# Kernel tuning notes

Measured on AMD Instinct MI355X. Metric: run time of the kernel, lower is better.

Reference implementation:

```python
import jax, jax.numpy as jnp
import numpy as np

N_SPECIES = 4
NUM_MODELS = 8
LAYER_DIMS = [384, 160, 128, 96, 1]
CELU_ALPHA = 0.1
N_ATOMS = 50000  # divisible by N_SPECIES -> balanced routing


def setup_inputs() -> dict:
    key = jax.random.key(0)
    ks = jax.random.split(key, 2 + 2 * (len(LAYER_DIMS) - 1))
    # Balanced species assignment: exactly N_ATOMS/N_SPECIES atoms per species,
    # randomly permuted (mirrors a real molecule's scattered per-species atoms
    # while keeping per-species group sizes static for jit).
    base = jnp.tile(jnp.arange(N_SPECIES, dtype=jnp.int64), N_ATOMS // N_SPECIES)
    species = jax.random.permutation(ks[0], base)[None, :]  # [1, N_ATOMS]
    aev = jax.random.normal(ks[1], (1, N_ATOMS, LAYER_DIMS[0]), dtype=jnp.float32)
    inp = {"species": species, "aev": aev}
    # Fused ensemble params per species: W [S, M, in, out], b [S, M, 1, out]
    for li in range(len(LAYER_DIMS) - 1):
        fin, fout = LAYER_DIMS[li], LAYER_DIMS[li + 1]
        scale = 1.0 / np.sqrt(fin)
        inp[f"W{li+1}"] = jax.random.uniform(
            ks[2 + 2 * li], (N_SPECIES, NUM_MODELS, fin, fout),
            dtype=jnp.float32, minval=-scale, maxval=scale)
        inp[f"b{li+1}"] = jax.random.uniform(
            ks[3 + 2 * li], (N_SPECIES, NUM_MODELS, 1, fout),
            dtype=jnp.float32, minval=-scale, maxval=scale)
    return inp


def _ensemble_mlp(x, W1, b1, W2, b2, W3, b3, W4, b4):
    # x: [S, n, F] routed atoms per species; W: [S, M, fin, fout]; b: [S, M, 1, fout]
    celu = lambda h: jax.nn.celu(h, alpha=CELU_ALPHA)
    h = celu(jnp.einsum('snf,smfo->smno', x, W1) + b1)   # [S, M, n, 160]
    h = celu(jnp.einsum('smnf,smfo->smno', h, W2) + b2)  # [S, M, n, 128]
    h = celu(jnp.einsum('smnf,smfo->smno', h, W3) + b3)  # [S, M, n, 96]
    h = jnp.einsum('smnf,smfo->smno', h, W4) + b4        # [S, M, n, 1]
    return h.mean(axis=1)                                 # mean over models -> [S, n, 1]


def reference(species, aev, W1, b1, W2, b2, W3, b3, W4, b4):
    n_atoms = species.shape[1]
    n_per = n_atoms // N_SPECIES
    # species-routed gather: stable argsort groups atoms by species; counts are
    # static (balanced) so reshape into [S, n_per] groups (== per-species index_select)
    order = jnp.argsort(species.reshape(-1), stable=True)
    x = aev.reshape(n_atoms, -1)[order].reshape(N_SPECIES, n_per, -1)
    atom_e = _ensemble_mlp(x, W1, b1, W2, b2, W3, b3, W4, b4)  # [S, n_per, 1]
    mol_energies = jnp.sum(atom_e).reshape(1)  # scatter-sum over all atoms/species
    return mol_energies
```

## Files before the change

kernel.cpp:

```cpp
#include <hip/hip_runtime.h>


#define NSP 4
#define NMODELS 8
#define MSPLIT 2
#define MPB (NMODELS / MSPLIT)
#define NATOMS 50000
#define NPER (NATOMS / NSP)
#define D0 384
#define D1 160
#define D2 128
#define D3 96
#define NRBLK ((NATOMS + 255) / 256)
#define ABLK 128
#define BPS ((NPER + ABLK - 1) / ABLK)
#define FRAGS_SM 184
#define CHUNKS_M 23
#define TOT_CHUNKS (MPB * CHUNKS_M)

typedef float f32x4 __attribute__((ext_vector_type(4)));
typedef __bf16 bf16x8 __attribute__((ext_vector_type(8)));

#define MFMA16(a, b, c) __builtin_amdgcn_mfma_f32_16x16x32_bf16((a), (b), (c), 0, 0, 0)

#define PALL_BYTES ((size_t)NSP * NMODELS * FRAGS_SM * 1024)
#define PBIAS_OFF PALL_BYTES
#define PBIAS_BYTES ((size_t)NSP * NMODELS * 512 * 2)
#define ORDER_OFF (PBIAS_OFF + PBIAS_BYTES)
#define BCNT_OFF (ORDER_OFF + (size_t)NATOMS * 4)
#define BPFX_OFF (BCNT_OFF + (size_t)NRBLK * NSP * 4)
#define BASE_OFF (BPFX_OFF + (size_t)NRBLK * NSP * 4)

static __device__ __forceinline__ unsigned short bfbits(float f) {
  __bf16 h = (__bf16)f;
  return __builtin_bit_cast(unsigned short, h);
}

static __device__ __forceinline__ float celu01(float x) {
  return fmaxf(x, 0.f) + 0.1f * fminf(0.f, __expf(x * 10.f) - 1.f);
}

static __device__ __forceinline__ void gload16(const void* g, void* l) {
  __builtin_amdgcn_global_load_lds(
      (const __attribute__((address_space(1))) unsigned int*)g,
      (__attribute__((address_space(3))) unsigned int*)l, 16, 0, 0);
}

__global__ __launch_bounds__(256) void count_kernel(const int* __restrict__ species,
                                                    int* __restrict__ bcnt) {
  __shared__ int cnt[NSP];
  int t = threadIdx.x;
  if (t < NSP) cnt[t] = 0;
  __syncthreads();
  int i = blockIdx.x * 256 + t;
  if (i < NATOMS) atomicAdd(&cnt[species[i]], 1);
  __syncthreads();
  if (t < NSP) bcnt[blockIdx.x * NSP + t] = cnt[t];
}

__global__ __launch_bounds__(256) void scan_kernel(const int* __restrict__ bcnt,
                                                   int* __restrict__ bpfx,
                                                   int* __restrict__ base) {
  int w = threadIdx.x >> 6;
  int lane = threadIdx.x & 63;
  __shared__ int totals[NSP];
  int carry = 0;
  for (int c = 0; c < (NRBLK + 63) / 64; ++c) {
    int idx = c * 64 + lane;
    int v = (idx < NRBLK) ? bcnt[idx * NSP + w] : 0;
    int incl = v;
    for (int off = 1; off < 64; off <<= 1) {
      int tv = __shfl_up(incl, off);
      if (lane >= off) incl += tv;
    }
    if (idx < NRBLK) bpfx[idx * NSP + w] = carry + incl - v;
    carry += __shfl(incl, 63);
  }
  if (lane == 0) totals[w] = carry;
  __syncthreads();
  if (threadIdx.x == 0) {
    int run = 0;
    for (int s = 0; s < NSP; ++s) { base[s] = run; run += totals[s]; }
  }
}

__global__ __launch_bounds__(256) void route_kernel(const int* __restrict__ species,
                                                    const int* __restrict__ bpfx,
                                                    const int* __restrict__ base,
                                                    int* __restrict__ order) {
  __shared__ int sp[256];
  int t = threadIdx.x;
  int i = blockIdx.x * 256 + t;
  sp[t] = (i < NATOMS) ? species[i] : -1;
  __syncthreads();
  if (i < NATOMS) {
    int s = sp[t];
    int rank = 0;
    for (int j = 0; j < t; ++j) rank += (sp[j] == s) ? 1 : 0;
    order[base[s] + bpfx[blockIdx.x * NSP + s] + rank] = i;
  }
}

__global__ __launch_bounds__(256) void pack_kernel(const float* __restrict__ W,
                                                   unsigned* __restrict__ dst,
                                                   int K, int N, int NT, int fragBase,
                                                   int total) {
  int tid = blockIdx.x * 256 + threadIdx.x;
  if (tid >= total) return;
  int per_sm = K * N / 2;
  int smi = tid / per_sm;
  int rem = tid - smi * per_sm;
  int frag = rem >> 8;
  int wi = rem & 255;
  int l = wi >> 2, d = wi & 3;
  int kf = frag / NT;
  int nt = frag - kf * NT;
  int k = kf * 32 + ((l >> 4) << 3) + 2 * d;
  int n = nt * 16 + (l & 15);
  const float* p = W + ((size_t)smi * K + k) * N + n;
  unsigned lo = bfbits(p[0]);
  unsigned hi = bfbits(p[N]);
  dst[((size_t)smi * FRAGS_SM + fragBase + frag) * 256 + wi] = lo | (hi << 16);
}

__global__ __launch_bounds__(256) void param_pack(const float* __restrict__ b1,
                                                  const float* __restrict__ b2,
                                                  const float* __restrict__ b3,
                                                  const float* __restrict__ W4,
                                                  const float* __restrict__ b4,
                                                  unsigned short* __restrict__ dst) {
  int i = blockIdx.x * 256 + threadIdx.x;
  if (i >= NSP * NMODELS * 512) return;
  int smi = i >> 9, o = i & 511;
  unsigned short v = 0;
  if (o < 160) v = bfbits(b1[smi * 160 + o]);
  else if (o < 288) v = bfbits(b2[smi * 128 + (o - 160)]);
  else if (o < 384) v = bfbits(b3[smi * 96 + (o - 288)]);
  else if (o < 480) v = bfbits(W4[smi * 96 + (o - 384)]);
  else if (o < 482) {
    unsigned u = __builtin_bit_cast(unsigned, b4[smi]);
    v = (unsigned short)((o == 480) ? (u & 0xffffu) : (u >> 16));
  }
  dst[i] = v;
}

__global__ __launch_bounds__(256, 2) void mlp_kernel(
    const float* __restrict__ aev, const int* __restrict__ order,
    const unsigned short* __restrict__ pAll, const unsigned short* __restrict__ pPar,
    float* __restrict__ out) {
  __shared__ alignas(16) unsigned short stage[2][4096];
  __shared__ alignas(16) __bf16 hbuf[4][32][168];
  __shared__ alignas(16) unsigned short hpar[MPB * 512];

  const int nwg = NSP * BPS * MSPLIT;
  const int cpx = nwg / 8;
  const int blk = (blockIdx.x % 8) * cpx + blockIdx.x / 8;
  const int s = blk / (BPS * MSPLIT);
  const int rem = blk - s * (BPS * MSPLIT);
  const int mh = rem / BPS;
  const int sb = rem - mh * BPS;
  const int tid = threadIdx.x;
  const int w = tid >> 6;
  const int l = tid & 63;
  const int l15 = l & 15;
  const int l4 = l >> 4;

  {
    const int4* src = (const int4*)(pPar + ((size_t)(s * NMODELS + mh * MPB)) * 512);
    ((int4*)hpar)[tid] = src[tid];
  }

  const size_t smBase = (size_t)(s * NMODELS + mh * MPB) * FRAGS_SM;
  const char* wsrc = (const char*)pAll + smBase * 1024 + (size_t)w * 2048 + (size_t)l * 16;

  bf16x8 a1[2][12];
#pragma unroll
  for (int mt = 0; mt < 2; ++mt) {
    int slot = sb * ABLK + w * 32 + mt * 16 + l15;
    int g = (slot < NPER) ? order[s * NPER + slot] : -1;
    if (g >= 0) {
      const float* rp = aev + (size_t)g * D0 + l4 * 8;
#pragma unroll
      for (int kf = 0; kf < 12; ++kf) {
        const float4* q = (const float4*)(rp + kf * 32);
        float4 lo = q[0], hi = q[1];
        bf16x8 f;
        f[0] = (__bf16)lo.x; f[1] = (__bf16)lo.y; f[2] = (__bf16)lo.z; f[3] = (__bf16)lo.w;
        f[4] = (__bf16)hi.x; f[5] = (__bf16)hi.y; f[6] = (__bf16)hi.z; f[7] = (__bf16)hi.w;
        a1[mt][kf] = f;
      }
    } else {
#pragma unroll
      for (int kf = 0; kf < 12; ++kf) {
        bf16x8 z;
#pragma unroll
        for (int e = 0; e < 8; ++e) z[e] = (__bf16)0.f;
        a1[mt][kf] = z;
      }
    }
  }

  const __bf16* hb = (const __bf16*)hpar;
  float acc4[2][4] = {{0.f, 0.f, 0.f, 0.f}, {0.f, 0.f, 0.f, 0.f}};
  float bbacc = 0.f;

  {
    char* d = (char*)stage + w * 2048;
    gload16(wsrc, d);
    gload16(wsrc + 1024, d + 1024);
  }
  __syncthreads();

  auto stage_next = [&](int gn) {
    if (gn < TOT_CHUNKS) {
      char* d = (char*)stage + (gn & 1) * 8192 + w * 2048;
      const char* src = wsrc + (size_t)gn * 8192;
      gload16(src, d);
      gload16(src + 1024, d + 1024);
    }
  };

  int gc = 0;

#pragma unroll 1
  for (int m = 0; m < MPB; ++m) {
    f32x4 C[2][10];

#pragma unroll
    for (int mt = 0; mt < 2; ++mt)
#pragma unroll
      for (int nt = 0; nt < 10; ++nt) {
        f32x4 z; z[0] = z[1] = z[2] = z[3] = 0.f; C[mt][nt] = z;
      }
#pragma unroll
    for (int c = 0; c < 15; ++c) {
      stage_next(gc + 1);
      const bf16x8* sbuf = (const bf16x8*)((const char*)stage + (gc & 1) * 8192);
#pragma unroll
      for (int j = 0; j < 8; ++j) {
        const int f = c * 8 + j;
        bf16x8 b = sbuf[j * 64 + l];
        C[0][f % 10] = MFMA16(a1[0][f / 10], b, C[0][f % 10]);
        C[1][f % 10] = MFMA16(a1[1][f / 10], b, C[1][f % 10]);
      }
      __syncthreads();
      ++gc;
    }
#pragma unroll
    for (int nt = 0; nt < 10; ++nt) {
      float bias = (float)hb[m * 512 + nt * 16 + l15];
#pragma unroll
      for (int mt = 0; mt < 2; ++mt)
#pragma unroll
        for (int r = 0; r < 4; ++r)
          hbuf[w][mt * 16 + l4 * 4 + r][nt * 16 + l15] = (__bf16)celu01(C[mt][nt][r] + bias);
    }

    bf16x8 a2[2][5];
#pragma unroll
    for (int mt = 0; mt < 2; ++mt)
#pragma unroll
      for (int kf = 0; kf < 5; ++kf)
        a2[mt][kf] = *(const bf16x8*)&hbuf[w][mt * 16 + l15][kf * 32 + l4 * 8];

#pragma unroll
    for (int mt = 0; mt < 2; ++mt)
#pragma unroll
      for (int nt = 0; nt < 8; ++nt) {
        f32x4 z; z[0] = z[1] = z[2] = z[3] = 0.f; C[mt][nt] = z;
      }
#pragma unroll
    for (int lc = 0; lc < 5; ++lc) {
      stage_next(gc + 1);
      const bf16x8* sbuf = (const bf16x8*)((const char*)stage + (gc & 1) * 8192);
#pragma unroll
      for (int j = 0; j < 8; ++j) {
        bf16x8 b = sbuf[j * 64 + l];
        C[0][j] = MFMA16(a2[0][lc], b, C[0][j]);
        C[1][j] = MFMA16(a2[1][lc], b, C[1][j]);
      }
      __syncthreads();
      ++gc;
    }
#pragma unroll
    for (int nt = 0; nt < 8; ++nt) {
      float bias = (float)hb[m * 512 + 160 + nt * 16 + l15];
#pragma unroll
      for (int mt = 0; mt < 2; ++mt)
#pragma unroll
        for (int r = 0; r < 4; ++r)
          hbuf[w][mt * 16 + l4 * 4 + r][nt * 16 + l15] = (__bf16)celu01(C[mt][nt][r] + bias);
    }

    bf16x8 a3[2][4];
#pragma unroll
    for (int mt = 0; mt < 2; ++mt)
#pragma unroll
      for (int kf = 0; kf < 4; ++kf)
        a3[mt][kf] = *(const bf16x8*)&hbuf[w][mt * 16 + l15][kf * 32 + l4 * 8];

#pragma unroll
    for (int mt = 0; mt < 2; ++mt)
#pragma unroll
      for (int nt = 0; nt < 6; ++nt) {
        f32x4 z; z[0] = z[1] = z[2] = z[3] = 0.f; C[mt][nt] = z;
      }
#pragma unroll
    for (int lc = 0; lc < 3; ++lc) {
      stage_next(gc + 1);
      const bf16x8* sbuf = (const bf16x8*)((const char*)stage + (gc & 1) * 8192);
#pragma unroll
      for (int j = 0; j < 8; ++j) {
        const int f = lc * 8 + j;
        bf16x8 b = sbuf[j * 64 + l];
        C[0][f % 6] = MFMA16(a3[0][f / 6], b, C[0][f % 6]);
        C[1][f % 6] = MFMA16(a3[1][f / 6], b, C[1][f % 6]);
      }
      __syncthreads();
      ++gc;
    }

    float e[2][4] = {{0.f, 0.f, 0.f, 0.f}, {0.f, 0.f, 0.f, 0.f}};
#pragma unroll
    for (int nt = 0; nt < 6; ++nt) {
      float b3v = (float)hb[m * 512 + 288 + nt * 16 + l15];
      float w4v = (float)hb[m * 512 + 384 + nt * 16 + l15];
#pragma unroll
      for (int mt = 0; mt < 2; ++mt)
#pragma unroll
        for (int r = 0; r < 4; ++r)
          e[mt][r] += celu01(C[mt][nt][r] + b3v) * w4v;
    }
#pragma unroll
    for (int mt = 0; mt < 2; ++mt)
#pragma unroll
      for (int r = 0; r < 4; ++r) acc4[mt][r] += e[mt][r];
    bbacc += ((const float*)hpar)[m * 256 + 240];
  }

  float tot = 0.f;
#pragma unroll
  for (int mt = 0; mt < 2; ++mt)
#pragma unroll
    for (int r = 0; r < 4; ++r) {
      float v = acc4[mt][r];
      v += __shfl_xor(v, 1);
      v += __shfl_xor(v, 2);
      v += __shfl_xor(v, 4);
      v += __shfl_xor(v, 8);
      int slot = sb * ABLK + w * 32 + mt * 16 + l4 * 4 + r;
      if (l15 == 0 && slot < NPER) tot += v + bbacc;
    }
  tot *= (1.f / NMODELS);
#pragma unroll
  for (int off = 1; off < 64; off <<= 1) tot += __shfl_xor(tot, off);
  if (l == 0) atomicAdd(out, tot);
}

extern "C" void kernel_launch(void* const* d_in, const int* in_sizes, int n_in,
                              void* d_out, int out_size, void* d_ws, size_t ws_size,
                              hipStream_t stream) {
  (void)in_sizes; (void)n_in; (void)out_size; (void)ws_size;
  const int* species = (const int*)d_in[0];
  const float* aev = (const float*)d_in[1];
  const float* W1 = (const float*)d_in[2];
  const float* b1 = (const float*)d_in[3];
  const float* W2 = (const float*)d_in[4];
  const float* b2 = (const float*)d_in[5];
  const float* W3 = (const float*)d_in[6];
  const float* b3 = (const float*)d_in[7];
  const float* W4 = (const float*)d_in[8];
  const float* b4 = (const float*)d_in[9];
  float* out = (float*)d_out;
  char* ws = (char*)d_ws;

  unsigned short* pAll = (unsigned short*)ws;
  unsigned short* pPar = (unsigned short*)(ws + PBIAS_OFF);
  int* order = (int*)(ws + ORDER_OFF);
  int* bcnt = (int*)(ws + BCNT_OFF);
  int* bpfx = (int*)(ws + BPFX_OFF);
  int* base = (int*)(ws + BASE_OFF);

  hipMemsetAsync(d_out, 0, sizeof(float), stream);

  count_kernel<<<NRBLK, 256, 0, stream>>>(species, bcnt);
  scan_kernel<<<1, 256, 0, stream>>>(bcnt, bpfx, base);
  route_kernel<<<NRBLK, 256, 0, stream>>>(species, bpfx, base, order);

  {
    int total = NSP * NMODELS * D0 * D1 / 2;
    pack_kernel<<<(total + 255) / 256, 256, 0, stream>>>(W1, (unsigned*)pAll, D0, D1, D1 / 16, 0, total);
  }
  {
    int total = NSP * NMODELS * D1 * D2 / 2;
    pack_kernel<<<(total + 255) / 256, 256, 0, stream>>>(W2, (unsigned*)pAll, D1, D2, D2 / 16, 120, total);
  }
  {
    int total = NSP * NMODELS * D2 * D3 / 2;
    pack_kernel<<<(total + 255) / 256, 256, 0, stream>>>(W3, (unsigned*)pAll, D2, D3, D3 / 16, 160, total);
  }
  {
    int total = NSP * NMODELS * 512;
    param_pack<<<(total + 255) / 256, 256, 0, stream>>>(b1, b2, b3, W4, b4, pPar);
  }

  mlp_kernel<<<NSP * BPS * MSPLIT, 256, 0, stream>>>(aev, order, pAll, pPar, out);
}
```

Baseline: 226.1 us.

## Split each layer's output columns in halves to cut registers and raise occupancy

Each layer's matmul is now computed in two passes over halves of the output columns. This halves the accumulator register footprint, so launch bounds can ask for 3 workgroups per CU instead of 2. The weight staging chunk is halved (4 KB double buffer) and the weights are repacked per column-half to match, doubling the chunk count and the number of barriers. The LDS copy of bias and params is removed in favour of direct global loads, which trades LDS space for extra scattered global reads. More launches of the pack kernel are also added.

```diff
diff --git a/kernel.cpp b/kernel.cpp
--- a/kernel.cpp
+++ b/kernel.cpp
@@ -15,7 +15,7 @@
 #define ABLK 128
 #define BPS ((NPER + ABLK - 1) / ABLK)
 #define FRAGS_SM 184
-#define CHUNKS_M 23
+#define CHUNKS_M 46
 #define TOT_CHUNKS (MPB * CHUNKS_M)
 
 typedef float f32x4 __attribute__((ext_vector_type(4)));
@@ -103,11 +103,12 @@
 
 __global__ __launch_bounds__(256) void pack_kernel(const float* __restrict__ W,
                                                    unsigned* __restrict__ dst,
-                                                   int K, int N, int NT, int fragBase,
+                                                   int K, int Nstride, int NT,
+                                                   int colBase, int fragBase,
                                                    int total) {
   int tid = blockIdx.x * 256 + threadIdx.x;
   if (tid >= total) return;
-  int per_sm = K * N / 2;
+  int per_sm = K * NT * 8;
   int smi = tid / per_sm;
   int rem = tid - smi * per_sm;
   int frag = rem >> 8;
@@ -116,10 +117,10 @@
   int kf = frag / NT;
   int nt = frag - kf * NT;
   int k = kf * 32 + ((l >> 4) << 3) + 2 * d;
-  int n = nt * 16 + (l & 15);
-  const float* p = W + ((size_t)smi * K + k) * N + n;
+  int n = colBase + nt * 16 + (l & 15);
+  const float* p = W + ((size_t)smi * K + k) * Nstride + n;
   unsigned lo = bfbits(p[0]);
-  unsigned hi = bfbits(p[N]);
+  unsigned hi = bfbits(p[Nstride]);
   dst[((size_t)smi * FRAGS_SM + fragBase + frag) * 256 + wi] = lo | (hi << 16);
 }
 
@@ -144,13 +145,12 @@
   dst[i] = v;
 }
 
-__global__ __launch_bounds__(256, 2) void mlp_kernel(
+__global__ __launch_bounds__(256, 3) void mlp_kernel(
     const float* __restrict__ aev, const int* __restrict__ order,
     const unsigned short* __restrict__ pAll, const unsigned short* __restrict__ pPar,
     float* __restrict__ out) {
-  __shared__ alignas(16) unsigned short stage[2][4096];
+  __shared__ alignas(16) unsigned short stage[2][2048];
   __shared__ alignas(16) __bf16 hbuf[4][32][168];
-  __shared__ alignas(16) unsigned short hpar[MPB * 512];
 
   const int nwg = NSP * BPS * MSPLIT;
   const int cpx = nwg / 8;
@@ -165,13 +165,13 @@
   const int l15 = l & 15;
   const int l4 = l >> 4;
 
-  {
-    const int4* src = (const int4*)(pPar + ((size_t)(s * NMODELS + mh * MPB)) * 512);
-    ((int4*)hpar)[tid] = src[tid];
-  }
-
   const size_t smBase = (size_t)(s * NMODELS + mh * MPB) * FRAGS_SM;
-  const char* wsrc = (const char*)pAll + smBase * 1024 + (size_t)w * 2048 + (size_t)l * 16;
+  const char* wsrc = (const char*)pAll + smBase * 1024 + (size_t)w * 1024 + (size_t)l * 16;
+
+  const unsigned short* parBf = pPar + (size_t)(s * NMODELS + mh * MPB) * 512;
+  auto ldbf = [&](int off) -> float {
+    return (float)__builtin_bit_cast(__bf16, parBf[off]);
+  };
 
   bf16x8 a1[2][12];
 #pragma unroll
@@ -200,60 +200,55 @@
     }
   }
 
-  const __bf16* hb = (const __bf16*)hpar;
   float acc4[2][4] = {{0.f, 0.f, 0.f, 0.f}, {0.f, 0.f, 0.f, 0.f}};
   float bbacc = 0.f;
 
-  {
-    char* d = (char*)stage + w * 2048;
-    gload16(wsrc, d);
-    gload16(wsrc + 1024, d + 1024);
-  }
+  gload16(wsrc, (char*)stage + w * 1024);
   __syncthreads();
 
   auto stage_next = [&](int gn) {
-    if (gn < TOT_CHUNKS) {
-      char* d = (char*)stage + (gn & 1) * 8192 + w * 2048;
-      const char* src = wsrc + (size_t)gn * 8192;
-      gload16(src, d);
-      gload16(src + 1024, d + 1024);
-    }
+    if (gn < TOT_CHUNKS)
+      gload16(wsrc + (size_t)gn * 4096,
+              (char*)stage + ((gn & 1) << 12) + w * 1024);
   };
 
   int gc = 0;
 
 #pragma unroll 1
   for (int m = 0; m < MPB; ++m) {
-    f32x4 C[2][10];
-
-#pragma unroll
-    for (int mt = 0; mt < 2; ++mt)
-#pragma unroll
-      for (int nt = 0; nt < 10; ++nt) {
-        f32x4 z; z[0] = z[1] = z[2] = z[3] = 0.f; C[mt][nt] = z;
-      }
-#pragma unroll
-    for (int c = 0; c < 15; ++c) {
-      stage_next(gc + 1);
-      const bf16x8* sbuf = (const bf16x8*)((const char*)stage + (gc & 1) * 8192);
-#pragma unroll
-      for (int j = 0; j < 8; ++j) {
-        const int f = c * 8 + j;
-        bf16x8 b = sbuf[j * 64 + l];
-        C[0][f % 10] = MFMA16(a1[0][f / 10], b, C[0][f % 10]);
-        C[1][f % 10] = MFMA16(a1[1][f / 10], b, C[1][f % 10]);
-      }
-      __syncthreads();
-      ++gc;
-    }
-#pragma unroll
-    for (int nt = 0; nt < 10; ++nt) {
-      float bias = (float)hb[m * 512 + nt * 16 + l15];
+#pragma unroll 1
+    for (int p = 0; p < 2; ++p) {
+      f32x4 C[2][5];
 #pragma unroll
       for (int mt = 0; mt < 2; ++mt)
 #pragma unroll
-        for (int r = 0; r < 4; ++r)
-          hbuf[w][mt * 16 + l4 * 4 + r][nt * 16 + l15] = (__bf16)celu01(C[mt][nt][r] + bias);
+        for (int nt = 0; nt < 5; ++nt) {
+          f32x4 z; z[0] = z[1] = z[2] = z[3] = 0.f; C[mt][nt] = z;
+        }
+#pragma unroll
+      for (int c = 0; c < 15; ++c) {
+        stage_next(gc + 1);
+        const bf16x8* sbuf = (const bf16x8*)((const char*)stage + ((gc & 1) << 12));
+#pragma unroll
+        for (int j = 0; j < 4; ++j) {
+          const int f = c * 4 + j;
+          bf16x8 b = sbuf[j * 64 + l];
+          C[0][f % 5] = MFMA16(a1[0][f / 5], b, C[0][f % 5]);
+          C[1][f % 5] = MFMA16(a1[1][f / 5], b, C[1][f % 5]);
+        }
+        __syncthreads();
+        ++gc;
+      }
+#pragma unroll
+      for (int nt = 0; nt < 5; ++nt) {
+        float bias = ldbf(m * 512 + p * 80 + nt * 16 + l15);
+#pragma unroll
+        for (int mt = 0; mt < 2; ++mt)
+#pragma unroll
+          for (int r = 0; r < 4; ++r)
+            hbuf[w][mt * 16 + l4 * 4 + r][p * 80 + nt * 16 + l15] =
+                (__bf16)celu01(C[mt][nt][r] + bias);
+      }
     }
 
     bf16x8 a2[2][5];
@@ -263,33 +258,39 @@
       for (int kf = 0; kf < 5; ++kf)
         a2[mt][kf] = *(const bf16x8*)&hbuf[w][mt * 16 + l15][kf * 32 + l4 * 8];
 
-#pragma unroll
-    for (int mt = 0; mt < 2; ++mt)
-#pragma unroll
-      for (int nt = 0; nt < 8; ++nt) {
-        f32x4 z; z[0] = z[1] = z[2] = z[3] = 0.f; C[mt][nt] = z;
-      }
-#pragma unroll
-    for (int lc = 0; lc < 5; ++lc) {
-      stage_next(gc + 1);
-      const bf16x8* sbuf = (const bf16x8*)((const char*)stage + (gc & 1) * 8192);
-#pragma unroll
-      for (int j = 0; j < 8; ++j) {
-        bf16x8 b = sbuf[j * 64 + l];
-        C[0][j] = MFMA16(a2[0][lc], b, C[0][j]);
-        C[1][j] = MFMA16(a2[1][lc], b, C[1][j]);
-      }
-      __syncthreads();
-      ++gc;
-    }
-#pragma unroll
-    for (int nt = 0; nt < 8; ++nt) {
-      float bias = (float)hb[m * 512 + 160 + nt * 16 + l15];
+#pragma unroll 1
+    for (int p = 0; p < 2; ++p) {
+      f32x4 C[2][4];
 #pragma unroll
       for (int mt = 0; mt < 2; ++mt)
 #pragma unroll
-        for (int r = 0; r < 4; ++r)
-          hbuf[w][mt * 16 + l4 * 4 + r][nt * 16 + l15] = (__bf16)celu01(C[mt][nt][r] + bias);
+        for (int nt = 0; nt < 4; ++nt) {
+          f32x4 z; z[0] = z[1] = z[2] = z[3] = 0.f; C[mt][nt] = z;
+        }
+#pragma unroll
+      for (int c = 0; c < 5; ++c) {
+        stage_next(gc + 1);
+        const bf16x8* sbuf = (const bf16x8*)((const char*)stage + ((gc & 1) << 12));
+#pragma unroll
+        for (int j = 0; j < 4; ++j) {
+          const int f = c * 4 + j;
+          bf16x8 b = sbuf[j * 64 + l];
+          C[0][f % 4] = MFMA16(a2[0][f / 4], b, C[0][f % 4]);
+          C[1][f % 4] = MFMA16(a2[1][f / 4], b, C[1][f % 4]);
+        }
+        __syncthreads();
+        ++gc;
+      }
+#pragma unroll
+      for (int nt = 0; nt < 4; ++nt) {
+        float bias = ldbf(m * 512 + 160 + p * 64 + nt * 16 + l15);
+#pragma unroll
+        for (int mt = 0; mt < 2; ++mt)
+#pragma unroll
+          for (int r = 0; r < 4; ++r)
+            hbuf[w][mt * 16 + l4 * 4 + r][p * 64 + nt * 16 + l15] =
+                (__bf16)celu01(C[mt][nt][r] + bias);
+      }
     }
 
     bf16x8 a3[2][4];
@@ -299,43 +300,46 @@
       for (int kf = 0; kf < 4; ++kf)
         a3[mt][kf] = *(const bf16x8*)&hbuf[w][mt * 16 + l15][kf * 32 + l4 * 8];
 
+    float e[2][4] = {{0.f, 0.f, 0.f, 0.f}, {0.f, 0.f, 0.f, 0.f}};
+#pragma unroll 1
+    for (int p = 0; p < 2; ++p) {
+      f32x4 C[2][3];
+#pragma unroll
+      for (int mt = 0; mt < 2; ++mt)
+#pragma unroll
+        for (int nt = 0; nt < 3; ++nt) {
+          f32x4 z; z[0] = z[1] = z[2] = z[3] = 0.f; C[mt][nt] = z;
+        }
+#pragma unroll
+      for (int c = 0; c < 3; ++c) {
+        stage_next(gc + 1);
+        const bf16x8* sbuf = (const bf16x8*)((const char*)stage + ((gc & 1) << 12));
+#pragma unroll
+        for (int j = 0; j < 4; ++j) {
+          const int f = c * 4 + j;
+          bf16x8 b = sbuf[j * 64 + l];
+          C[0][f % 3] = MFMA16(a3[0][f / 3], b, C[0][f % 3]);
+          C[1][f % 3] = MFMA16(a3[1][f / 3], b, C[1][f % 3]);
+        }
+        __syncthreads();
+        ++gc;
+      }
+#pragma unroll
+      for (int nt = 0; nt < 3; ++nt) {
+        float b3v = ldbf(m * 512 + 288 + p * 48 + nt * 16 + l15);
+        float w4v = ldbf(m * 512 + 384 + p * 48 + nt * 16 + l15);
+#pragma unroll
+        for (int mt = 0; mt < 2; ++mt)
+#pragma unroll
+          for (int r = 0; r < 4; ++r)
+            e[mt][r] += celu01(C[mt][nt][r] + b3v) * w4v;
+      }
+    }
 #pragma unroll
     for (int mt = 0; mt < 2; ++mt)
 #pragma unroll
-      for (int nt = 0; nt < 6; ++nt) {
-        f32x4 z; z[0] = z[1] = z[2] = z[3] = 0.f; C[mt][nt] = z;
-      }
-#pragma unroll
-    for (int lc = 0; lc < 3; ++lc) {
-      stage_next(gc + 1);
-      const bf16x8* sbuf = (const bf16x8*)((const char*)stage + (gc & 1) * 8192);
-#pragma unroll
-      for (int j = 0; j < 8; ++j) {
-        const int f = lc * 8 + j;
-        bf16x8 b = sbuf[j * 64 + l];
-        C[0][f % 6] = MFMA16(a3[0][f / 6], b, C[0][f % 6]);
-        C[1][f % 6] = MFMA16(a3[1][f / 6], b, C[1][f % 6]);
-      }
-      __syncthreads();
-      ++gc;
-    }
-
-    float e[2][4] = {{0.f, 0.f, 0.f, 0.f}, {0.f, 0.f, 0.f, 0.f}};
-#pragma unroll
-    for (int nt = 0; nt < 6; ++nt) {
-      float b3v = (float)hb[m * 512 + 288 + nt * 16 + l15];
-      float w4v = (float)hb[m * 512 + 384 + nt * 16 + l15];
-#pragma unroll
-      for (int mt = 0; mt < 2; ++mt)
-#pragma unroll
-        for (int r = 0; r < 4; ++r)
-          e[mt][r] += celu01(C[mt][nt][r] + b3v) * w4v;
-    }
-#pragma unroll
-    for (int mt = 0; mt < 2; ++mt)
-#pragma unroll
       for (int r = 0; r < 4; ++r) acc4[mt][r] += e[mt][r];
-    bbacc += ((const float*)hpar)[m * 256 + 240];
+    bbacc += ((const float*)pPar)[(size_t)(s * NMODELS + mh * MPB + m) * 256 + 240];
   }
 
   float tot = 0.f;
@@ -388,16 +392,19 @@
   route_kernel<<<NRBLK, 256, 0, stream>>>(species, bpfx, base, order);
 
   {
-    int total = NSP * NMODELS * D0 * D1 / 2;
-    pack_kernel<<<(total + 255) / 256, 256, 0, stream>>>(W1, (unsigned*)pAll, D0, D1, D1 / 16, 0, total);
+    int total = NSP * NMODELS * D0 * 80 / 2;
+    pack_kernel<<<(total + 255) / 256, 256, 0, stream>>>(W1, (unsigned*)pAll, D0, D1, 5, 0, 0, total);
+    pack_kernel<<<(total + 255) / 256, 256, 0, stream>>>(W1, (unsigned*)pAll, D0, D1, 5, 80, 60, total);
   }
   {
-    int total = NSP * NMODELS * D1 * D2 / 2;
-    pack_kernel<<<(total + 255) / 256, 256, 0, stream>>>(W2, (unsigned*)pAll, D1, D2, D2 / 16, 120, total);
+    int total = NSP * NMODELS * D1 * 64 / 2;
+    pack_kernel<<<(total + 255) / 256, 256, 0, stream>>>(W2, (unsigned*)pAll, D1, D2, 4, 0, 120, total);
+    pack_kernel<<<(total + 255) / 256, 256, 0, stream>>>(W2, (unsigned*)pAll, D1, D2, 4, 64, 140, total);
   }
   {
-    int total = NSP * NMODELS * D2 * D3 / 2;
-    pack_kernel<<<(total + 255) / 256, 256, 0, stream>>>(W3, (unsigned*)pAll, D2, D3, D3 / 16, 160, total);
+    int total = NSP * NMODELS * D2 * 48 / 2;
+    pack_kernel<<<(total + 255) / 256, 256, 0, stream>>>(W3, (unsigned*)pAll, D2, D3, 3, 0, 160, total);
+    pack_kernel<<<(total + 255) / 256, 256, 0, stream>>>(W3, (unsigned*)pAll, D2, D3, 3, 48, 172, total);
   }
   {
     int total = NSP * NMODELS * 512;
```

After: 317.5 us. +40.4%, slower.

## Swap MFMA operands to pass activations via register shuffles and prepack AEV

Applied to the files above, without the earlier changes.

The MLP kernel now treats weights as the A operand and activations as the B operand. Inter-layer activations are redistributed with wave shuffles instead of round-tripping through an LDS buffer. A new pre-kernel gathers the routed AEV rows into bf16 MFMA-fragment layout, so the main kernel streams layer-1 activations per K-fragment instead of holding all 12 in registers. Dropping the LDS hbuf and hpar and cutting register pressure allows 3 blocks per CU instead of 2. The cost is an extra gather kernel, a workspace round trip for AEV, and bias reads from global memory.

```diff
diff --git a/kernel.cpp b/kernel.cpp
--- a/kernel.cpp
+++ b/kernel.cpp
@@ -7,6 +7,8 @@
 #define MPB (NMODELS / MSPLIT)
 #define NATOMS 50000
 #define NPER (NATOMS / NSP)
+#define NPAD 12544
+#define NG16 (NPAD / 16)
 #define D0 384
 #define D1 160
 #define D2 128
@@ -17,6 +19,7 @@
 #define FRAGS_SM 184
 #define CHUNKS_M 23
 #define TOT_CHUNKS (MPB * CHUNKS_M)
+#define MAXKF(c) ((8 * (c) + 7) / 10)
 
 typedef float f32x4 __attribute__((ext_vector_type(4)));
 typedef __bf16 bf16x8 __attribute__((ext_vector_type(8)));
@@ -30,10 +33,16 @@
 #define BCNT_OFF (ORDER_OFF + (size_t)NATOMS * 4)
 #define BPFX_OFF (BCNT_OFF + (size_t)NRBLK * NSP * 4)
 #define BASE_OFF (BPFX_OFF + (size_t)NRBLK * NSP * 4)
+#define AEVF_OFF (BASE_OFF + 1024)
+#define AEVF_BYTES ((size_t)NSP * NG16 * 12 * 1024)
 
 static __device__ __forceinline__ unsigned short bfbits(float f) {
   __bf16 h = (__bf16)f;
   return __builtin_bit_cast(unsigned short, h);
+}
+
+static __device__ __forceinline__ float bf2f(unsigned short u) {
+  return (float)__builtin_bit_cast(__bf16, u);
 }
 
 static __device__ __forceinline__ float celu01(float x) {
@@ -99,6 +108,33 @@
     for (int j = 0; j < t; ++j) rank += (sp[j] == s) ? 1 : 0;
     order[base[s] + bpfx[blockIdx.x * NSP + s] + rank] = i;
   }
+}
+
+__global__ __launch_bounds__(256) void aev_pack(const float* __restrict__ aev,
+                                                const int* __restrict__ order,
+                                                unsigned short* __restrict__ aevf) {
+  int tid = blockIdx.x * 256 + threadIdx.x;
+  int frag = tid >> 6;
+  int l = tid & 63;
+  if (frag >= NSP * NG16 * 12) return;
+  int s = frag / (NG16 * 12);
+  int r2 = frag - s * (NG16 * 12);
+  int g16 = r2 / 12;
+  int kf = r2 - g16 * 12;
+  int slot = g16 * 16 + (l & 15);
+  int k0 = kf * 32 + (l >> 4) * 8;
+  unsigned short o[8];
+  if (slot < NPER) {
+    int src = order[s * NPER + slot];
+    const float4* q = (const float4*)(aev + (size_t)src * D0 + k0);
+    float4 v0 = q[0], v1 = q[1];
+    o[0] = bfbits(v0.x); o[1] = bfbits(v0.y); o[2] = bfbits(v0.z); o[3] = bfbits(v0.w);
+    o[4] = bfbits(v1.x); o[5] = bfbits(v1.y); o[6] = bfbits(v1.z); o[7] = bfbits(v1.w);
+  } else {
+#pragma unroll
+    for (int e = 0; e < 8; ++e) o[e] = 0;
+  }
+  *(int4*)(aevf + ((size_t)frag << 9) + l * 8) = *(const int4*)o;
 }
 
 __global__ __launch_bounds__(256) void pack_kernel(const float* __restrict__ W,
@@ -144,13 +180,11 @@
   dst[i] = v;
 }
 
-__global__ __launch_bounds__(256, 2) void mlp_kernel(
-    const float* __restrict__ aev, const int* __restrict__ order,
+__global__ __launch_bounds__(256, 3) void mlp_kernel(
+    const unsigned short* __restrict__ aevf,
     const unsigned short* __restrict__ pAll, const unsigned short* __restrict__ pPar,
     float* __restrict__ out) {
   __shared__ alignas(16) unsigned short stage[2][4096];
-  __shared__ alignas(16) __bf16 hbuf[4][32][168];
-  __shared__ alignas(16) unsigned short hpar[MPB * 512];
 
   const int nwg = NSP * BPS * MSPLIT;
   const int cpx = nwg / 8;
@@ -165,43 +199,23 @@
   const int l15 = l & 15;
   const int l4 = l >> 4;
 
-  {
-    const int4* src = (const int4*)(pPar + ((size_t)(s * NMODELS + mh * MPB)) * 512);
-    ((int4*)hpar)[tid] = src[tid];
-  }
-
   const size_t smBase = (size_t)(s * NMODELS + mh * MPB) * FRAGS_SM;
   const char* wsrc = (const char*)pAll + smBase * 1024 + (size_t)w * 2048 + (size_t)l * 16;
 
-  bf16x8 a1[2][12];
-#pragma unroll
-  for (int mt = 0; mt < 2; ++mt) {
-    int slot = sb * ABLK + w * 32 + mt * 16 + l15;
-    int g = (slot < NPER) ? order[s * NPER + slot] : -1;
-    if (g >= 0) {
-      const float* rp = aev + (size_t)g * D0 + l4 * 8;
-#pragma unroll
-      for (int kf = 0; kf < 12; ++kf) {
-        const float4* q = (const float4*)(rp + kf * 32);
-        float4 lo = q[0], hi = q[1];
-        bf16x8 f;
-        f[0] = (__bf16)lo.x; f[1] = (__bf16)lo.y; f[2] = (__bf16)lo.z; f[3] = (__bf16)lo.w;
-        f[4] = (__bf16)hi.x; f[5] = (__bf16)hi.y; f[6] = (__bf16)hi.z; f[7] = (__bf16)hi.w;
-        a1[mt][kf] = f;
-      }
-    } else {
-#pragma unroll
-      for (int kf = 0; kf < 12; ++kf) {
-        bf16x8 z;
-#pragma unroll
-        for (int e = 0; e < 8; ++e) z[e] = (__bf16)0.f;
-        a1[mt][kf] = z;
-      }
-    }
-  }
-
-  const __bf16* hb = (const __bf16*)hpar;
-  float acc4[2][4] = {{0.f, 0.f, 0.f, 0.f}, {0.f, 0.f, 0.f, 0.f}};
+  const size_t afr = ((size_t)s * NG16 + sb * 8 + w * 2) * 12;
+  auto ldB = [&](int mt, int kf) -> bf16x8 {
+    return *(const bf16x8*)(aevf + ((afr + (size_t)mt * 12 + kf) << 9) + l * 8);
+  };
+
+  const int src0 = ((l4 & 1) << 5) | l15;
+  const int src1 = src0 + 16;
+  const bool hiSel = (l4 & 2) != 0;
+
+  bf16x8 bw[2][2];
+  bw[0][0] = ldB(0, 0);
+  bw[1][0] = ldB(1, 0);
+
+  float accE[2] = {0.f, 0.f};
   float bbacc = 0.f;
 
   {
@@ -214,9 +228,9 @@
   auto stage_next = [&](int gn) {
     if (gn < TOT_CHUNKS) {
       char* d = (char*)stage + (gn & 1) * 8192 + w * 2048;
-      const char* src = wsrc + (size_t)gn * 8192;
-      gload16(src, d);
-      gload16(src + 1024, d + 1024);
+      const char* sp = wsrc + (size_t)gn * 8192;
+      gload16(sp, d);
+      gload16(sp + 1024, d + 1024);
     }
   };
 
@@ -224,133 +238,174 @@
 
 #pragma unroll 1
   for (int m = 0; m < MPB; ++m) {
-    f32x4 C[2][10];
-
+    const unsigned short* pb = pPar + (size_t)(s * NMODELS + mh * MPB + m) * 512;
+
+    f32x4 C1[2][10];
 #pragma unroll
     for (int mt = 0; mt < 2; ++mt)
 #pragma unroll
       for (int nt = 0; nt < 10; ++nt) {
-        f32x4 z; z[0] = z[1] = z[2] = z[3] = 0.f; C[mt][nt] = z;
+        f32x4 z; z[0] = z[1] = z[2] = z[3] = 0.f; C1[mt][nt] = z;
       }
 #pragma unroll
     for (int c = 0; c < 15; ++c) {
       stage_next(gc + 1);
+      if (c < 14 && MAXKF(c + 1) > MAXKF(c)) {
+        const int nk = MAXKF(c + 1);
+        bw[0][nk & 1] = ldB(0, nk);
+        bw[1][nk & 1] = ldB(1, nk);
+      }
       const bf16x8* sbuf = (const bf16x8*)((const char*)stage + (gc & 1) * 8192);
 #pragma unroll
       for (int j = 0; j < 8; ++j) {
         const int f = c * 8 + j;
-        bf16x8 b = sbuf[j * 64 + l];
-        C[0][f % 10] = MFMA16(a1[0][f / 10], b, C[0][f % 10]);
-        C[1][f % 10] = MFMA16(a1[1][f / 10], b, C[1][f % 10]);
+        bf16x8 wA = sbuf[j * 64 + l];
+        C1[0][f % 10] = MFMA16(wA, bw[0][(f / 10) & 1], C1[0][f % 10]);
+        C1[1][f % 10] = MFMA16(wA, bw[1][(f / 10) & 1], C1[1][f % 10]);
       }
       __syncthreads();
       ++gc;
     }
-#pragma unroll
-    for (int nt = 0; nt < 10; ++nt) {
-      float bias = (float)hb[m * 512 + nt * 16 + l15];
-#pragma unroll
-      for (int mt = 0; mt < 2; ++mt)
-#pragma unroll
-        for (int r = 0; r < 4; ++r)
-          hbuf[w][mt * 16 + l4 * 4 + r][nt * 16 + l15] = (__bf16)celu01(C[mt][nt][r] + bias);
-    }
-
-    bf16x8 a2[2][5];
+
+    bf16x8 b2[2][5];
+    {
+      ushort4 bv[10];
+#pragma unroll
+      for (int nt = 0; nt < 10; ++nt)
+        bv[nt] = *(const ushort4*)(pb + nt * 16 + (l4 << 2));
+#pragma unroll
+      for (int mt = 0; mt < 2; ++mt) {
+        unsigned pk[10][2];
+#pragma unroll
+        for (int nt = 0; nt < 10; ++nt) {
+          float h0 = celu01(C1[mt][nt][0] + bf2f(bv[nt].x));
+          float h1 = celu01(C1[mt][nt][1] + bf2f(bv[nt].y));
+          float h2 = celu01(C1[mt][nt][2] + bf2f(bv[nt].z));
+          float h3 = celu01(C1[mt][nt][3] + bf2f(bv[nt].w));
+          pk[nt][0] = (unsigned)bfbits(h0) | ((unsigned)bfbits(h1) << 16);
+          pk[nt][1] = (unsigned)bfbits(h2) | ((unsigned)bfbits(h3) << 16);
+        }
+#pragma unroll
+        for (int kf = 0; kf < 5; ++kf) {
+          int d0a = __shfl((int)pk[2 * kf][0], src0), d0b = __shfl((int)pk[2 * kf + 1][0], src0);
+          int d1a = __shfl((int)pk[2 * kf][1], src0), d1b = __shfl((int)pk[2 * kf + 1][1], src0);
+          int d2a = __shfl((int)pk[2 * kf][0], src1), d2b = __shfl((int)pk[2 * kf + 1][0], src1);
+          int d3a = __shfl((int)pk[2 * kf][1], src1), d3b = __shfl((int)pk[2 * kf + 1][1], src1);
+          int4 di;
+          di.x = hiSel ? d0b : d0a;
+          di.y = hiSel ? d1b : d1a;
+          di.z = hiSel ? d2b : d2a;
+          di.w = hiSel ? d3b : d3a;
+          b2[mt][kf] = __builtin_bit_cast(bf16x8, di);
+        }
+      }
+    }
+
+    f32x4 C2[2][8];
 #pragma unroll
     for (int mt = 0; mt < 2; ++mt)
 #pragma unroll
-      for (int kf = 0; kf < 5; ++kf)
-        a2[mt][kf] = *(const bf16x8*)&hbuf[w][mt * 16 + l15][kf * 32 + l4 * 8];
-
-#pragma unroll
-    for (int mt = 0; mt < 2; ++mt)
-#pragma unroll
       for (int nt = 0; nt < 8; ++nt) {
-        f32x4 z; z[0] = z[1] = z[2] = z[3] = 0.f; C[mt][nt] = z;
-      }
-#pragma unroll
-    for (int lc = 0; lc < 5; ++lc) {
+        f32x4 z; z[0] = z[1] = z[2] = z[3] = 0.f; C2[mt][nt] = z;
+      }
+#pragma unroll
+    for (int c2 = 0; c2 < 5; ++c2) {
       stage_next(gc + 1);
       const bf16x8* sbuf = (const bf16x8*)((const char*)stage + (gc & 1) * 8192);
 #pragma unroll
       for (int j = 0; j < 8; ++j) {
-        bf16x8 b = sbuf[j * 64 + l];
-        C[0][j] = MFMA16(a2[0][lc], b, C[0][j]);
-        C[1][j] = MFMA16(a2[1][lc], b, C[1][j]);
+        bf16x8 wA = sbuf[j * 64 + l];
+        C2[0][j] = MFMA16(wA, b2[0][c2], C2[0][j]);
+        C2[1][j] = MFMA16(wA, b2[1][c2], C2[1][j]);
       }
       __syncthreads();
       ++gc;
     }
-#pragma unroll
-    for (int nt = 0; nt < 8; ++nt) {
-      float bias = (float)hb[m * 512 + 160 + nt * 16 + l15];
-#pragma unroll
-      for (int mt = 0; mt < 2; ++mt)
-#pragma unroll
-        for (int r = 0; r < 4; ++r)
-          hbuf[w][mt * 16 + l4 * 4 + r][nt * 16 + l15] = (__bf16)celu01(C[mt][nt][r] + bias);
-    }
-
-    bf16x8 a3[2][4];
+
+    bf16x8 b3[2][4];
+    {
+      ushort4 bv[8];
+#pragma unroll
+      for (int nt = 0; nt < 8; ++nt)
+        bv[nt] = *(const ushort4*)(pb + 160 + nt * 16 + (l4 << 2));
+#pragma unroll
+      for (int mt = 0; mt < 2; ++mt) {
+        unsigned pk[8][2];
+#pragma unroll
+        for (int nt = 0; nt < 8; ++nt) {
+          float h0 = celu01(C2[mt][nt][0] + bf2f(bv[nt].x));
+          float h1 = celu01(C2[mt][nt][1] + bf2f(bv[nt].y));
+          float h2 = celu01(C2[mt][nt][2] + bf2f(bv[nt].z));
+          float h3 = celu01(C2[mt][nt][3] + bf2f(bv[nt].w));
+          pk[nt][0] = (unsigned)bfbits(h0) | ((unsigned)bfbits(h1) << 16);
+          pk[nt][1] = (unsigned)bfbits(h2) | ((unsigned)bfbits(h3) << 16);
+        }
+#pragma unroll
+        for (int kf = 0; kf < 4; ++kf) {
+          int d0a = __shfl((int)pk[2 * kf][0], src0), d0b = __shfl((int)pk[2 * kf + 1][0], src0);
+          int d1a = __shfl((int)pk[2 * kf][1], src0), d1b = __shfl((int)pk[2 * kf + 1][1], src0);
+          int d2a = __shfl((int)pk[2 * kf][0], src1), d2b = __shfl((int)pk[2 * kf + 1][0], src1);
+          int d3a = __shfl((int)pk[2 * kf][1], src1), d3b = __shfl((int)pk[2 * kf + 1][1], src1);
+          int4 di;
+          di.x = hiSel ? d0b : d0a;
+          di.y = hiSel ? d1b : d1a;
+          di.z = hiSel ? d2b : d2a;
+          di.w = hiSel ? d3b : d3a;
+          b3[mt][kf] = __builtin_bit_cast(bf16x8, di);
+        }
+      }
+    }
+
+    f32x4 C3[2][6];
 #pragma unroll
     for (int mt = 0; mt < 2; ++mt)
 #pragma unroll
-      for (int kf = 0; kf < 4; ++kf)
-        a3[mt][kf] = *(const bf16x8*)&hbuf[w][mt * 16 + l15][kf * 32 + l4 * 8];
-
-#pragma unroll
-    for (int mt = 0; mt < 2; ++mt)
-#pragma unroll
       for (int nt = 0; nt < 6; ++nt) {
-        f32x4 z; z[0] = z[1] = z[2] = z[3] = 0.f; C[mt][nt] = z;
+        f32x4 z; z[0] = z[1] = z[2] = z[3] = 0.f; C3[mt][nt] = z;
       }
 #pragma unroll
     for (int lc = 0; lc < 3; ++lc) {
       stage_next(gc + 1);
+      if (lc == 0) {
+        bw[0][0] = ldB(0, 0);
+        bw[1][0] = ldB(1, 0);
+      }
       const bf16x8* sbuf = (const bf16x8*)((const char*)stage + (gc & 1) * 8192);
 #pragma unroll
       for (int j = 0; j < 8; ++j) {
         const int f = lc * 8 + j;
-        bf16x8 b = sbuf[j * 64 + l];
-        C[0][f % 6] = MFMA16(a3[0][f / 6], b, C[0][f % 6]);
-        C[1][f % 6] = MFMA16(a3[1][f / 6], b, C[1][f % 6]);
+        bf16x8 wA = sbuf[j * 64 + l];
+        C3[0][f % 6] = MFMA16(wA, b3[0][f / 6], C3[0][f % 6]);
+        C3[1][f % 6] = MFMA16(wA, b3[1][f / 6], C3[1][f % 6]);
       }
       __syncthreads();
       ++gc;
     }
 
-    float e[2][4] = {{0.f, 0.f, 0.f, 0.f}, {0.f, 0.f, 0.f, 0.f}};
 #pragma unroll
     for (int nt = 0; nt < 6; ++nt) {
-      float b3v = (float)hb[m * 512 + 288 + nt * 16 + l15];
-      float w4v = (float)hb[m * 512 + 384 + nt * 16 + l15];
+      ushort4 b3v = *(const ushort4*)(pb + 288 + nt * 16 + (l4 << 2));
+      ushort4 w4v = *(const ushort4*)(pb + 384 + nt * 16 + (l4 << 2));
+      float bb[4] = {bf2f(b3v.x), bf2f(b3v.y), bf2f(b3v.z), bf2f(b3v.w)};
+      float ww[4] = {bf2f(w4v.x), bf2f(w4v.y), bf2f(w4v.z), bf2f(w4v.w)};
 #pragma unroll
       for (int mt = 0; mt < 2; ++mt)
 #pragma unroll
         for (int r = 0; r < 4; ++r)
-          e[mt][r] += celu01(C[mt][nt][r] + b3v) * w4v;
-    }
-#pragma unroll
-    for (int mt = 0; mt < 2; ++mt)
-#pragma unroll
-      for (int r = 0; r < 4; ++r) acc4[mt][r] += e[mt][r];
-    bbacc += ((const float*)hpar)[m * 256 + 240];
+          accE[mt] += celu01(C3[mt][nt][r] + bb[r]) * ww[r];
+    }
+    bbacc += ((const float*)pPar)[(size_t)(s * NMODELS + mh * MPB + m) * 256 + 240];
   }
 
   float tot = 0.f;
 #pragma unroll
-  for (int mt = 0; mt < 2; ++mt)
-#pragma unroll
-    for (int r = 0; r < 4; ++r) {
-      float v = acc4[mt][r];
-      v += __shfl_xor(v, 1);
-      v += __shfl_xor(v, 2);
-      v += __shfl_xor(v, 4);
-      v += __shfl_xor(v, 8);
-      int slot = sb * ABLK + w * 32 + mt * 16 + l4 * 4 + r;
-      if (l15 == 0 && slot < NPER) tot += v + bbacc;
-    }
+  for (int mt = 0; mt < 2; ++mt) {
+    float v = accE[mt];
+    v += __shfl_xor(v, 16);
+    v += __shfl_xor(v, 32);
+    int slot = sb * ABLK + w * 32 + mt * 16 + l15;
+    if (l < 16 && slot < NPER) tot += v + bbacc;
+  }
   tot *= (1.f / NMODELS);
 #pragma unroll
   for (int off = 1; off < 64; off <<= 1) tot += __shfl_xor(tot, off);
@@ -380,6 +435,7 @@
   int* bcnt = (int*)(ws + BCNT_OFF);
   int* bpfx = (int*)(ws + BPFX_OFF);
   int* base = (int*)(ws + BASE_OFF);
+  unsigned short* aevf = (unsigned short*)(ws + AEVF_OFF);
 
   hipMemsetAsync(d_out, 0, sizeof(float), stream);
 
@@ -388,6 +444,10 @@
   route_kernel<<<NRBLK, 256, 0, stream>>>(species, bpfx, base, order);
 
   {
+    int total = NSP * NG16 * 12 * 64;
+    aev_pack<<<(total + 255) / 256, 256, 0, stream>>>(aev, order, aevf);
+  }
+  {
     int total = NSP * NMODELS * D0 * D1 / 2;
     pack_kernel<<<(total + 255) / 256, 256, 0, stream>>>(W1, (unsigned*)pAll, D0, D1, D1 / 16, 0, total);
   }
@@ -404,5 +464,5 @@
     param_pack<<<(total + 255) / 256, 256, 0, stream>>>(b1, b2, b3, W4, b4, pPar);
   }
 
-  mlp_kernel<<<NSP * BPS * MSPLIT, 256, 0, stream>>>(aev, order, pAll, pPar, out);
-}
+  mlp_kernel<<<NSP * BPS * MSPLIT, 256, 0, stream>>>(aevf, pAll, pPar, out);
+}
```

Result: slower. 249.2 us (+10.2%).
